# Optimization experiments

Hardware: AMD Instinct MI355X
Metric: run time of the kernel (lower is better)

Reference implementation:

```python
import jax, jax.numpy as jnp
import numpy as np
from jax import lax

B = 64; C_IN = 3; HW = 64
D_INPUT = 256; D_MODEL = 1024; HEADS = 8; HEAD_DIM = D_INPUT // HEADS
ITERS = 16; MEM_LEN = 25; MEM_HID = 64
N_SYNCH = 256; OUT_DIMS = 1000
SYNCH_SIZE = N_SYNCH * (N_SYNCH + 1) // 2  # 32896
TRIU_I, TRIU_J = np.triu_indices(N_SYNCH)
EPS = 1e-5
SCALE = float(1.0 / np.sqrt(HEAD_DIM))


def setup_inputs() -> dict:
    key = jax.random.key(0)
    ks = iter(jax.random.split(key, 64))
    def rn(shape, scale=0.02):
        return jax.random.normal(next(ks), shape, jnp.float32) * scale
    inp = {
        'x': jax.random.normal(next(ks), (B, C_IN, HW, HW), jnp.float32),
        # backbone: conv(3->256) + BN, conv(256->256) + BN
        'conv1_w': rn((D_INPUT, C_IN, 3, 3)), 'conv1_b': jnp.zeros((D_INPUT,), jnp.float32),
        'bn1_g': jnp.ones((D_INPUT,), jnp.float32), 'bn1_b': jnp.zeros((D_INPUT,), jnp.float32),
        'conv2_w': rn((D_INPUT, D_INPUT, 3, 3)), 'conv2_b': jnp.zeros((D_INPUT,), jnp.float32),
        'bn2_g': jnp.ones((D_INPUT,), jnp.float32), 'bn2_b': jnp.zeros((D_INPUT,), jnp.float32),
        # kv projection + LayerNorm
        'kv_w': rn((D_INPUT, D_INPUT)), 'kv_b': jnp.zeros((D_INPUT,), jnp.float32),
        'ln_kv_g': jnp.ones((D_INPUT,), jnp.float32), 'ln_kv_b': jnp.zeros((D_INPUT,), jnp.float32),
        # q projection from action-synch representation
        'q_w': rn((SYNCH_SIZE, D_INPUT)), 'q_b': jnp.zeros((D_INPUT,), jnp.float32),
        # multihead attention in/out projections
        'wq': rn((D_INPUT, D_INPUT)), 'bq': jnp.zeros((D_INPUT,), jnp.float32),
        'wk': rn((D_INPUT, D_INPUT)), 'bk': jnp.zeros((D_INPUT,), jnp.float32),
        'wv': rn((D_INPUT, D_INPUT)), 'bv': jnp.zeros((D_INPUT,), jnp.float32),
        'wo': rn((D_INPUT, D_INPUT)), 'bo_p': jnp.zeros((D_INPUT,), jnp.float32),
        # synapses: Linear(d_input+d_model -> 2*d_model) + GLU + LayerNorm
        'syn_w': rn((D_INPUT + D_MODEL, 2 * D_MODEL)), 'syn_b': jnp.zeros((2 * D_MODEL,), jnp.float32),
        'ln_syn_g': jnp.ones((D_MODEL,), jnp.float32), 'ln_syn_b': jnp.zeros((D_MODEL,), jnp.float32),
        # trace processor (per-neuron SuperLinear MLPs)
        'tp1_w': rn((MEM_LEN, 2 * MEM_HID, D_MODEL), 0.1), 'tp1_b': jnp.zeros((1, D_MODEL, 2 * MEM_HID), jnp.float32),
        'tp2_w': rn((MEM_HID, 2, D_MODEL), 0.1), 'tp2_b': jnp.zeros((1, D_MODEL, 2), jnp.float32),
        # output projector
        'out_w': rn((SYNCH_SIZE, OUT_DIMS)), 'out_b': jnp.zeros((OUT_DIMS,), jnp.float32),
        # recurrent initial state + decay params
        'start_act': rn((D_MODEL,), 0.03), 'start_trace': rn((D_MODEL, MEM_LEN), 0.03),
        'decay_a': jax.random.uniform(next(ks), (SYNCH_SIZE,), jnp.float32) * 0.5,
        'decay_o': jax.random.uniform(next(ks), (SYNCH_SIZE,), jnp.float32) * 0.5,
    }
    return inp


def _conv(x, w, b):
    y = lax.conv_general_dilated(x, w, (1, 1), 'SAME', dimension_numbers=('NCHW', 'OIHW', 'NCHW'))
    return y + b[None, :, None, None]

def _pool(x):
    return lax.reduce_window(x, -jnp.inf, lax.max, (1, 1, 2, 2), (1, 1, 2, 2), 'VALID')

def _bn(x, g, b):
    m = x.mean((0, 2, 3), keepdims=True)
    v = ((x - m) ** 2).mean((0, 2, 3), keepdims=True)
    return g[None, :, None, None] * (x - m) * lax.rsqrt(v + EPS) + b[None, :, None, None]

def _ln(x, g, b):
    m = x.mean(-1, keepdims=True)
    v = ((x - m) ** 2).mean(-1, keepdims=True)
    return g * (x - m) * lax.rsqrt(v + EPS) + b

def _glu(t):
    a, g = jnp.split(t, 2, axis=-1)
    return a * jax.nn.sigmoid(g)

def _synch(sel, alpha, beta, r):
    # outer[:, i, j] == sel[:, i] * sel[:, j] for upper-triangular (i, j)
    pp = sel[:, TRIU_I] * sel[:, TRIU_J]
    alpha = r * alpha + pp
    beta = r * beta + 1.0
    return alpha * lax.rsqrt(beta), alpha, beta


def reference(x, conv1_w, conv1_b, bn1_g, bn1_b, conv2_w, conv2_b, bn2_g, bn2_b,
              kv_w, kv_b, ln_kv_g, ln_kv_b, q_w, q_b, wq, bq, wk, bk, wv, bv, wo, bo_p,
              syn_w, syn_b, ln_syn_g, ln_syn_b, tp1_w, tp1_b, tp2_w, tp2_b,
              out_w, out_b, start_act, start_trace, decay_a, decay_o):
    # backbone -> kv features [B, S, D_INPUT], S = 16*16
    h = _pool(jax.nn.relu(_bn(_conv(x, conv1_w, conv1_b), bn1_g, bn1_b)))
    h = _pool(jax.nn.relu(_bn(_conv(h, conv2_w, conv2_b), bn2_g, bn2_b)))
    feat = h.reshape(B, D_INPUT, -1).transpose(0, 2, 1)
    kv = _ln(feat @ kv_w + kv_b, ln_kv_g, ln_kv_b)
    kh = (kv @ wk + bk).reshape(B, -1, HEADS, HEAD_DIM)
    vh = (kv @ wv + bv).reshape(B, -1, HEADS, HEAD_DIM)

    r_a = jnp.exp(-decay_a)[None]
    r_o = jnp.exp(-decay_o)[None]
    act0 = jnp.broadcast_to(start_act, (B, D_MODEL))
    trace0 = jnp.broadcast_to(start_trace, (B, D_MODEL, MEM_LEN))
    sel0 = act0[:, :N_SYNCH]
    ao0 = sel0[:, TRIU_I] * sel0[:, TRIU_J]
    bo0 = jnp.ones_like(ao0)
    aa0 = jnp.zeros((B, SYNCH_SIZE), x.dtype)  # r*0 + pp reproduces the None-init branch
    ba0 = jnp.zeros((B, SYNCH_SIZE), x.dtype)
    so0 = jnp.zeros((B, SYNCH_SIZE), x.dtype)

    def step(carry, _):
        trace, act, aa, ba, ao, bo, _so = carry
        sa, aa, ba = _synch(act[:, -N_SYNCH:], aa, ba, r_a)
        q = sa @ q_w + q_b
        qh = (q @ wq + bq).reshape(B, HEADS, HEAD_DIM)
        scores = jnp.einsum('bhd,bshd->bhs', qh, kh) * SCALE
        w = jax.nn.softmax(scores, axis=-1)
        attn = jnp.einsum('bhs,bshd->bhd', w, vh).reshape(B, D_INPUT) @ wo + bo_p
        pre = jnp.concatenate([attn, act], axis=-1)
        state = _ln(_glu(pre @ syn_w + syn_b), ln_syn_g, ln_syn_b)
        trace = jnp.concatenate([trace[:, :, 1:], state[:, :, None]], axis=-1)
        hmid = _glu(jnp.einsum('bdm,mhd->bdh', trace, tp1_w) + tp1_b)  # [B, D, MEM_HID]
        act = _glu(jnp.einsum('bdm,mhd->bdh', hmid, tp2_w) + tp2_b)[..., 0]  # [B, D]
        so, ao, bo = _synch(act[:, :N_SYNCH], ao, bo, r_o)
        pred = so @ out_w + out_b
        lp = jax.nn.log_softmax(pred, axis=-1)
        ne = -(jnp.exp(lp) * lp).sum(-1) / jnp.log(jnp.float32(OUT_DIMS))
        cert = jnp.stack([ne, 1.0 - ne], axis=-1)
        return (trace, act, aa, ba, ao, bo, so), (pred, cert)

    carry, (preds, certs) = lax.scan(step, (trace0, act0, aa0, ba0, ao0, bo0, so0), None, length=ITERS)
    predictions = jnp.transpose(preds, (1, 2, 0))   # [B, OUT_DIMS, ITERS]
    certainties = jnp.transpose(certs, (1, 2, 0))   # [B, 2, ITERS]
    return predictions, certainties, carry[6]
```

## Files before the change

### kernel.cpp

```cpp
#include <hip/hip_runtime.h>

#define SYNCH 32896
#define EPS 1e-5f

__device__ __forceinline__ float wave_sum(float v) {
#pragma unroll
  for (int o = 32; o; o >>= 1) v += __shfl_xor(v, o, 64);
  return v;
}
__device__ __forceinline__ float wave_max(float v) {
#pragma unroll
  for (int o = 32; o; o >>= 1) v = fmaxf(v, __shfl_xor(v, o, 64));
  return v;
}
__device__ __forceinline__ float block_sum(float v, float* red, int t) {
  v = wave_sum(v);
  __syncthreads();
  if ((t & 63) == 0) red[t >> 6] = v;
  __syncthreads();
  return red[0] + red[1] + red[2] + red[3];
}
__device__ __forceinline__ float block_max(float v, float* red, int t) {
  v = wave_max(v);
  __syncthreads();
  if ((t & 63) == 0) red[t >> 6] = v;
  __syncthreads();
  return fmaxf(fmaxf(red[0], red[1]), fmaxf(red[2], red[3]));
}
__device__ __forceinline__ float sigm(float x) { return 1.f / (1.f + __expf(-x)); }

__device__ __forceinline__ float conv1_at(const float* __restrict__ x,
                                          const float* __restrict__ w,
                                          int b, int o, int y, int xx) {
  float acc = 0.f;
#pragma unroll
  for (int c = 0; c < 3; ++c) {
    const float* xp = x + ((b * 3 + c) << 12);
    const float* wp = w + (o * 3 + c) * 9;
#pragma unroll
    for (int ky = 0; ky < 3; ++ky) {
      int iy = y + ky - 1;
      if ((unsigned)iy > 63u) continue;
#pragma unroll
      for (int kx = 0; kx < 3; ++kx) {
        int ix = xx + kx - 1;
        if ((unsigned)ix > 63u) continue;
        acc += xp[(iy << 6) + ix] * wp[ky * 3 + kx];
      }
    }
  }
  return acc;
}

__global__ __launch_bounds__(256) void conv1_stats_k(const float* __restrict__ x,
    const float* __restrict__ w, const float* __restrict__ bias, float* __restrict__ st) {
  int idx = blockIdx.x * 256 + threadIdx.x;
  int xx = idx & 63, yy = (idx >> 6) & 63, o = (idx >> 12) & 255, b = idx >> 20;
  float v = bias[o] + conv1_at(x, w, b, o, yy, xx);
  __shared__ float red[4];
  float s = block_sum(v, red, threadIdx.x);
  float s2 = block_sum(v * v, red, threadIdx.x);
  if (threadIdx.x == 0) { atomicAdd(&st[o], s); atomicAdd(&st[256 + o], s2); }
}

__global__ void bn_final_k(const float* st, float* m, float* inv, float n) {
  int o = threadIdx.x;
  float mu = st[o] / n;
  float var = st[256 + o] / n - mu * mu;
  m[o] = mu; inv[o] = rsqrtf(var + EPS);
}

__global__ __launch_bounds__(256) void conv1_pool_k(const float* __restrict__ x,
    const float* __restrict__ w, const float* __restrict__ bias,
    const float* __restrict__ m, const float* __restrict__ inv,
    const float* __restrict__ g, const float* __restrict__ bb,
    float* __restrict__ h1) {
  int idx = blockIdx.x * 256 + threadIdx.x;
  int xx = idx & 31, yy = (idx >> 5) & 31, o = (idx >> 10) & 255, b = idx >> 18;
  float mu = m[o], iv = inv[o], gg = g[o], be = bb[o], bi = bias[o];
  float best = -1e30f;
#pragma unroll
  for (int py = 0; py < 2; ++py)
#pragma unroll
    for (int px = 0; px < 2; ++px) {
      float v = bi + conv1_at(x, w, b, o, 2 * yy + py, 2 * xx + px);
      v = fmaxf(gg * (v - mu) * iv + be, 0.f);
      best = fmaxf(best, v);
    }
  h1[((b * 256 + o) * 32 + yy) * 32 + xx] = best;
}

__global__ __launch_bounds__(256) void conv2_k(const float* __restrict__ h1,
    const float* __restrict__ w, const float* __restrict__ bias, float* __restrict__ y2) {
  __shared__ __align__(16) float tile[34 * 36];
  int b = blockIdx.x >> 4;
  int og = blockIdx.x & 15;
  int t = threadIdx.x;
  int o = og * 16 + (t >> 4);
  int l = t & 15;
  int x0 = (l & 3) * 8, y0 = (l >> 2) * 8;
  float acc[8][8];
#pragma unroll
  for (int i = 0; i < 8; ++i)
#pragma unroll
    for (int j = 0; j < 8; ++j) acc[i][j] = 0.f;
  for (int c = 0; c < 256; ++c) {
    __syncthreads();
    for (int i = t; i < 34 * 34; i += 256) {
      int r = i / 34, cc = i - r * 34;
      int iy = r - 1, ix = cc - 1;
      float v = 0.f;
      if ((unsigned)iy < 32u && (unsigned)ix < 32u) v = h1[((b * 256 + c) * 32 + iy) * 32 + ix];
      tile[r * 36 + cc] = v;
    }
    __syncthreads();
    const float* wp = w + (o * 256 + c) * 9;
    float w0 = wp[0], w1 = wp[1], w2 = wp[2], w3 = wp[3], w4 = wp[4],
          w5 = wp[5], w6 = wp[6], w7 = wp[7], w8 = wp[8];
#pragma unroll
    for (int r = 0; r < 10; ++r) {
      const float* trow = &tile[(y0 + r) * 36 + x0];
      float4 A = *(const float4*)trow;
      float4 Bq = *(const float4*)(trow + 4);
      float4 Cq = *(const float4*)(trow + 8);
      float v[12] = {A.x, A.y, A.z, A.w, Bq.x, Bq.y, Bq.z, Bq.w, Cq.x, Cq.y, Cq.z, Cq.w};
#pragma unroll
      for (int i = 0; i < 8; ++i) {
        int ky = r - i;
        if (ky < 0 || ky > 2) continue;
        float wk0 = (ky == 0) ? w0 : (ky == 1) ? w3 : w6;
        float wk1 = (ky == 0) ? w1 : (ky == 1) ? w4 : w7;
        float wk2 = (ky == 0) ? w2 : (ky == 1) ? w5 : w8;
#pragma unroll
        for (int j = 0; j < 8; ++j)
          acc[i][j] += v[j] * wk0 + v[j + 1] * wk1 + v[j + 2] * wk2;
      }
    }
  }
  float bo = bias[o];
#pragma unroll
  for (int i = 0; i < 8; ++i)
#pragma unroll
    for (int j = 0; j < 8; ++j)
      y2[((b * 256 + o) * 32 + y0 + i) * 32 + x0 + j] = acc[i][j] + bo;
}

__global__ __launch_bounds__(256) void bn2_stats_k(const float* __restrict__ y2,
    float* __restrict__ m2, float* __restrict__ i2) {
  int o = blockIdx.x, t = threadIdx.x;
  float s = 0.f, s2 = 0.f;
  for (int i = t; i < 65536; i += 256) {
    int b = i >> 10, sp = i & 1023;
    float v = y2[((b << 8) + o) * 1024 + sp];
    s += v; s2 += v * v;
  }
  __shared__ float red[4];
  float S = block_sum(s, red, t);
  float S2 = block_sum(s2, red, t);
  if (t == 0) {
    float mu = S / 65536.f;
    m2[o] = mu;
    i2[o] = rsqrtf(S2 / 65536.f - mu * mu + EPS);
  }
}

__global__ __launch_bounds__(256) void pool2_k(const float* __restrict__ y2,
    const float* __restrict__ m2, const float* __restrict__ i2,
    const float* __restrict__ g, const float* __restrict__ bb, float* __restrict__ feat) {
  int idx = blockIdx.x * 256 + threadIdx.x;
  int d = idx & 255, s = (idx >> 8) & 255, b = idx >> 16;
  int yy = s >> 4, xx = s & 15;
  const float* base = y2 + ((size_t)(b * 256 + d) << 10);
  float mu = m2[d], iv = i2[d], gg = g[d], be = bb[d];
  float best = -1e30f;
#pragma unroll
  for (int py = 0; py < 2; ++py)
#pragma unroll
    for (int px = 0; px < 2; ++px) {
      float v = base[(2 * yy + py) * 32 + 2 * xx + px];
      v = fmaxf(gg * (v - mu) * iv + be, 0.f);
      best = fmaxf(best, v);
    }
  feat[(b * 256 + s) * 256 + d] = best;
}

__global__ __launch_bounds__(256) void gemm4x4_k(const float* __restrict__ A, int lda,
    const float* __restrict__ A2, int lda2, int K1,
    const float* __restrict__ W, const float* __restrict__ bias,
    float* __restrict__ C, int M, int N, int K, int kchunk, int atomic) {
  __shared__ __align__(16) float As[16][68];
  __shared__ __align__(16) float Ws[16][68];
  int tx = threadIdx.x, ty = threadIdx.y;
  int tid = ty * 16 + tx;
  int n0 = blockIdx.x * 64, m0 = blockIdx.y * 64;
  int k_lo = blockIdx.z * kchunk;
  int k_hi = min(K, k_lo + kchunk);
  float acc[4][4];
#pragma unroll
  for (int i = 0; i < 4; ++i)
#pragma unroll
    for (int j = 0; j < 4; ++j) acc[i][j] = 0.f;
  for (int k0 = k_lo; k0 < k_hi; k0 += 16) {
    __syncthreads();
#pragma unroll
    for (int q = 0; q < 4; ++q) {
      int r = (tid >> 4) + q * 16, c = tid & 15;
      int mm = m0 + r, kk = k0 + c;
      float a = 0.f;
      if (mm < M && kk < k_hi) a = (kk < K1) ? A[mm * lda + kk] : A2[mm * lda2 + kk - K1];
      As[c][r] = a;
    }
#pragma unroll
    for (int q = 0; q < 4; ++q) {
      int kk = (tid >> 6) + q * 4, nn = tid & 63;
      int kg = k0 + kk, n = n0 + nn;
      Ws[kk][nn] = (kg < k_hi && n < N) ? W[kg * N + n] : 0.f;
    }
    __syncthreads();
#pragma unroll
    for (int kk = 0; kk < 16; ++kk) {
      float4 av = *(const float4*)&As[kk][ty * 4];
      float4 wv = *(const float4*)&Ws[kk][tx * 4];
      float av4[4] = {av.x, av.y, av.z, av.w};
      float wv4[4] = {wv.x, wv.y, wv.z, wv.w};
#pragma unroll
      for (int i = 0; i < 4; ++i)
#pragma unroll
        for (int j = 0; j < 4; ++j) acc[i][j] += av4[i] * wv4[j];
    }
  }
#pragma unroll
  for (int i = 0; i < 4; ++i) {
    int mm = m0 + ty * 4 + i;
    if (mm >= M) continue;
#pragma unroll
    for (int j = 0; j < 4; ++j) {
      int n = n0 + tx * 4 + j;
      if (n >= N) continue;
      float v = acc[i][j];
      if (bias && blockIdx.z == 0) v += bias[n];
      if (atomic) atomicAdd(&C[mm * N + n], v);
      else C[mm * N + n] = v;
    }
  }
}

__global__ __launch_bounds__(256) void ln256_k(float* __restrict__ x,
    const float* __restrict__ g, const float* __restrict__ b) {
  int row = blockIdx.x, t = threadIdx.x;
  float v = x[row * 256 + t];
  __shared__ float red[4];
  float mu = block_sum(v, red, t) * (1.f / 256.f);
  float d = v - mu;
  float var = block_sum(d * d, red, t) * (1.f / 256.f);
  float rs = rsqrtf(var + EPS);
  x[row * 256 + t] = g[t] * d * rs + b[t];
}

__global__ __launch_bounds__(256) void skinny_k(const float* __restrict__ AT,
    const float* __restrict__ W, float* __restrict__ part, int K, int N, int kchunk) {
  int n = blockIdx.x * 256 + threadIdx.x;
  int nc = min(n, N - 1);
  int kc = blockIdx.y;
  int k_lo = kc * kchunk, k_hi = min(K, k_lo + kchunk);
  float acc[64];
#pragma unroll
  for (int b = 0; b < 64; ++b) acc[b] = 0.f;
  for (int k = k_lo; k < k_hi; ++k) {
    float w = W[k * N + nc];
    const float* __restrict__ ap = AT + (k << 6);
#pragma unroll
    for (int b = 0; b < 64; ++b) acc[b] += ap[b] * w;
  }
  if (n < N) {
#pragma unroll
    for (int b = 0; b < 64; ++b) part[(kc * 64 + b) * N + n] = acc[b];
  }
}

__global__ __launch_bounds__(256) void skred_k(const float* __restrict__ part,
    const float* __restrict__ bias, float* __restrict__ C, int N, int nch) {
  int n = blockIdx.x * 256 + threadIdx.x;
  int b = blockIdx.y;
  if (n >= N) return;
  float s = bias[n];
  for (int kc = 0; kc < nch; ++kc) s += part[(kc * 64 + b) * N + n];
  C[b * N + n] = s;
}

__global__ __launch_bounds__(256) void attn_k(const float* __restrict__ qh,
    const float* __restrict__ kh, const float* __restrict__ vh, float* __restrict__ out) {
  int b = blockIdx.x >> 3, h = blockIdx.x & 7;
  int t = threadIdx.x;
  __shared__ float qs[32];
  __shared__ float wgt[256];
  __shared__ float pv[256];
  __shared__ float red[4];
  if (t < 32) qs[t] = qh[b * 256 + h * 32 + t];
  __syncthreads();
  const float4* kp = (const float4*)(kh + ((size_t)((b * 256 + t) * 8 + h)) * 32);
  float sc = 0.f;
#pragma unroll
  for (int q = 0; q < 8; ++q) {
    float4 k4 = kp[q];
    sc += k4.x * qs[4 * q] + k4.y * qs[4 * q + 1] + k4.z * qs[4 * q + 2] + k4.w * qs[4 * q + 3];
  }
  sc *= 0.17677669529663687f;
  float M = block_max(sc, red, t);
  float e = __expf(sc - M);
  float S = block_sum(e, red, t);
  wgt[t] = e / S;
  __syncthreads();
  int d = t & 31, grp = t >> 5;
  float a = 0.f;
  for (int s = grp; s < 256; s += 8)
    a += wgt[s] * vh[((size_t)((b * 256 + s) * 8 + h)) * 32 + d];
  pv[t] = a;
  __syncthreads();
  if (t < 32) {
    float s = 0.f;
#pragma unroll
    for (int g2 = 0; g2 < 8; ++g2) s += pv[g2 * 32 + t];
    out[b * 256 + h * 32 + t] = s;
  }
}

__global__ __launch_bounds__(256) void gluln_k(const float* __restrict__ gt,
    const float* __restrict__ g, const float* __restrict__ bb,
    float* __restrict__ trace, int slot) {
  int b = blockIdx.x, t = threadIdx.x;
  float v[4];
  float s = 0.f;
#pragma unroll
  for (int i = 0; i < 4; ++i) {
    int d = i * 256 + t;
    float a = gt[b * 2048 + d];
    float gg = gt[b * 2048 + 1024 + d];
    v[i] = a * sigm(gg);
    s += v[i];
  }
  __shared__ float red[4];
  float mu = block_sum(s, red, t) * (1.f / 1024.f);
  float s2 = 0.f;
#pragma unroll
  for (int i = 0; i < 4; ++i) { float d0 = v[i] - mu; s2 += d0 * d0; }
  float var = block_sum(s2, red, t) * (1.f / 1024.f);
  float rs = rsqrtf(var + EPS);
  float* tr = trace + (b * 25 + slot) * 1024;
#pragma unroll
  for (int i = 0; i < 4; ++i) {
    int d = i * 256 + t;
    tr[d] = g[d] * (v[i] - mu) * rs + bb[d];
  }
}

#define FMA4(dst, sv, wv) dst.x += sv.x*wv.x; dst.y += sv.y*wv.y; dst.z += sv.z*wv.z; dst.w += sv.w*wv.w;
__global__ __launch_bounds__(256) void tp1_k(const float* __restrict__ trace,
    const float* __restrict__ w1, const float* __restrict__ b1,
    float* __restrict__ hmid, int toff) {
  int gx = blockIdx.x * 256 + threadIdx.x;
  int d4 = gx & 255;
  int hg = (gx >> 8) & 7;
  int bp = gx >> 11;
  int b0 = bp * 2;
  int h0 = hg * 8;
  float4 acc[2][2][8];
#pragma unroll
  for (int a = 0; a < 2; ++a)
#pragma unroll
    for (int c = 0; c < 2; ++c)
#pragma unroll
      for (int u = 0; u < 8; ++u) acc[a][c][u] = make_float4(0.f, 0.f, 0.f, 0.f);
  for (int m = 0; m < 25; ++m) {
    int pm = toff + m; if (pm >= 25) pm -= 25;
    float4 t0 = *(const float4*)&trace[((b0) * 25 + pm) * 1024 + d4 * 4];
    float4 t1 = *(const float4*)&trace[((b0 + 1) * 25 + pm) * 1024 + d4 * 4];
    const float* wb = w1 + m * 131072 + d4 * 4;
#pragma unroll
    for (int u = 0; u < 8; ++u) {
      float4 wa = *(const float4*)&wb[(h0 + u) * 1024];
      float4 wg = *(const float4*)&wb[(64 + h0 + u) * 1024];
      FMA4(acc[0][0][u], t0, wa); FMA4(acc[0][1][u], t0, wg);
      FMA4(acc[1][0][u], t1, wa); FMA4(acc[1][1][u], t1, wg);
    }
  }
  int dbase = d4 * 4;
#pragma unroll
  for (int u = 0; u < 8; ++u) {
    int h = h0 + u;
#pragma unroll
    for (int bb2 = 0; bb2 < 2; ++bb2) {
      float4 av = acc[bb2][0][u], gv = acc[bb2][1][u];
      av.x += b1[(dbase + 0) * 128 + h];      av.y += b1[(dbase + 1) * 128 + h];
      av.z += b1[(dbase + 2) * 128 + h];      av.w += b1[(dbase + 3) * 128 + h];
      gv.x += b1[(dbase + 0) * 128 + 64 + h]; gv.y += b1[(dbase + 1) * 128 + 64 + h];
      gv.z += b1[(dbase + 2) * 128 + 64 + h]; gv.w += b1[(dbase + 3) * 128 + 64 + h];
      float4 hm;
      hm.x = av.x * sigm(gv.x); hm.y = av.y * sigm(gv.y);
      hm.z = av.z * sigm(gv.z); hm.w = av.w * sigm(gv.w);
      *(float4*)&hmid[((b0 + bb2) * 64 + h) * 1024 + dbase] = hm;
    }
  }
}

__global__ __launch_bounds__(256) void tp2_k(const float* __restrict__ hmid,
    const float* __restrict__ w2, const float* __restrict__ b2, float* __restrict__ act) {
  int gx = blockIdx.x * 256 + threadIdx.x;
  int d = gx & 1023, b = gx >> 10;
  float a = b2[d * 2], gg = b2[d * 2 + 1];
  for (int h = 0; h < 64; ++h) {
    float hm = hmid[(b * 64 + h) * 1024 + d];
    a += hm * w2[(h * 2) * 1024 + d];
    gg += hm * w2[(h * 2 + 1) * 1024 + d];
  }
  act[gx] = a * sigm(gg);
}

__global__ void selT_k(const float* __restrict__ act, float* __restrict__ selT, int off) {
  int gx = blockIdx.x * 256 + threadIdx.x;
  int b = gx & 63, i = gx >> 6;
  selT[gx] = act[b * 1024 + off + i];
}

__global__ __launch_bounds__(256) void synch_k(const float* __restrict__ selT,
    const int* __restrict__ I, const int* __restrict__ J, const float* __restrict__ r,
    float* __restrict__ al, float* __restrict__ be, float* __restrict__ outT) {
  int gx = blockIdx.x * 256 + threadIdx.x;
  int b = gx & 63, p = gx >> 6;
  float pp = selT[(I[p] << 6) + b] * selT[(J[p] << 6) + b];
  float rr = r[p];
  float a = rr * al[gx] + pp;
  float bt = rr * be[gx] + 1.f;
  al[gx] = a; be[gx] = bt;
  outT[gx] = a * rsqrtf(bt);
}

__global__ __launch_bounds__(256) void entropy_k(const float* __restrict__ pred,
    float* __restrict__ dout, int t) {
  int b = blockIdx.x, tid = threadIdx.x;
  __shared__ float sp[1000];
  __shared__ float red[4];
  float mx = -1e30f;
  for (int i = tid; i < 1000; i += 256) {
    float v = pred[b * 1000 + i];
    sp[i] = v;
    mx = fmaxf(mx, v);
  }
  float M = block_max(mx, red, tid);
  float se = 0.f;
  for (int i = tid; i < 1000; i += 256) se += __expf(sp[i] - M);
  float S = block_sum(se, red, tid);
  float lse = M + __logf(S);
  float acc = 0.f;
  for (int i = tid; i < 1000; i += 256) {
    float lp = sp[i] - lse;
    acc += __expf(lp) * lp;
    dout[b * 16000 + i * 16 + t] = sp[i];
  }
  float E = block_sum(acc, red, tid);
  if (tid == 0) {
    float ne = -E * (1.f / 6.907755278982137f);
    dout[1024000 + b * 32 + t] = ne;
    dout[1024000 + b * 32 + 16 + t] = 1.f - ne;
  }
}

__global__ void triu_k(int* __restrict__ I, int* __restrict__ J) {
  int p = blockIdx.x * 256 + threadIdx.x;
  if (p >= SYNCH) return;
  float pf = (float)p;
  int i = (int)floorf((513.f - sqrtf(513.f * 513.f - 8.f * pf)) * 0.5f);
  i = max(0, min(255, i));
  while (i > 0 && i * (513 - i) / 2 > p) --i;
  while (i < 255 && (i + 1) * (513 - (i + 1)) / 2 <= p) ++i;
  I[p] = i;
  J[p] = i + (p - i * (513 - i) / 2);
}

__global__ void initr_k(const float* da, const float* dc, float* ra, float* ro) {
  int p = blockIdx.x * 256 + threadIdx.x;
  if (p >= SYNCH) return;
  ra[p] = __expf(-da[p]);
  ro[p] = __expf(-dc[p]);
}

__global__ void initact_k(const float* sa, float* act) {
  int gx = blockIdx.x * 256 + threadIdx.x;
  act[gx] = sa[gx & 1023];
}

__global__ void inittrace_k(const float* st, float* trace) {
  int r = blockIdx.x * 256 + threadIdx.x;
  int b = blockIdx.y;
  int m = r >> 10, d = r & 1023;
  trace[(b * 25 + m) * 1024 + d] = st[d * 25 + m];
}

__global__ void initsynch_k(const int* __restrict__ I, const int* __restrict__ J,
    const float* __restrict__ sa, float* aa, float* ba, float* ao, float* bo) {
  int gx = blockIdx.x * 256 + threadIdx.x;
  int p = gx >> 6;
  aa[gx] = 0.f; ba[gx] = 0.f;
  ao[gx] = sa[I[p]] * sa[J[p]];
  bo[gx] = 1.f;
}

__global__ void soout_k(const float* __restrict__ soT, float* __restrict__ dout) {
  int p = blockIdx.x * 256 + threadIdx.x;
  int b = blockIdx.y;
  if (p >= SYNCH) return;
  dout[1026048 + b * 32896 + p] = soT[(p << 6) + b];
}

extern "C" void kernel_launch(void* const* d_in, const int* in_sizes, int n_in,
                              void* d_out, int out_size, void* d_ws, size_t ws_size,
                              hipStream_t stream) {
  (void)in_sizes; (void)n_in; (void)out_size; (void)ws_size;
  const float* x      = (const float*)d_in[0];
  const float* c1w    = (const float*)d_in[1];
  const float* c1b    = (const float*)d_in[2];
  const float* bn1g   = (const float*)d_in[3];
  const float* bn1b   = (const float*)d_in[4];
  const float* c2w    = (const float*)d_in[5];
  const float* c2b    = (const float*)d_in[6];
  const float* bn2g   = (const float*)d_in[7];
  const float* bn2b   = (const float*)d_in[8];
  const float* kvw    = (const float*)d_in[9];
  const float* kvb    = (const float*)d_in[10];
  const float* lnkvg  = (const float*)d_in[11];
  const float* lnkvb  = (const float*)d_in[12];
  const float* qw     = (const float*)d_in[13];
  const float* qb     = (const float*)d_in[14];
  const float* wq     = (const float*)d_in[15];
  const float* bq     = (const float*)d_in[16];
  const float* wk     = (const float*)d_in[17];
  const float* bk     = (const float*)d_in[18];
  const float* wv     = (const float*)d_in[19];
  const float* bv     = (const float*)d_in[20];
  const float* wo     = (const float*)d_in[21];
  const float* bop    = (const float*)d_in[22];
  const float* synw   = (const float*)d_in[23];
  const float* synb   = (const float*)d_in[24];
  const float* lnsg   = (const float*)d_in[25];
  const float* lnsb   = (const float*)d_in[26];
  const float* t1w    = (const float*)d_in[27];
  const float* t1b    = (const float*)d_in[28];
  const float* t2w    = (const float*)d_in[29];
  const float* t2b    = (const float*)d_in[30];
  const float* outw   = (const float*)d_in[31];
  const float* outb   = (const float*)d_in[32];
  const float* sact   = (const float*)d_in[33];
  const float* strace = (const float*)d_in[34];
  const float* dca    = (const float*)d_in[35];
  const float* dco    = (const float*)d_in[36];
  float* out = (float*)d_out;

  float* W = (float*)d_ws;
  size_t off = 0;
  auto alloc = [&](size_t n) { float* p = W + off; off += (n + 63) & ~(size_t)63; return p; };
  float* h1    = alloc(16777216);
  float* y2    = alloc(16777216);
  float* feat  = alloc(4194304);
  float* kv    = alloc(4194304);
  float* kh    = alloc(4194304);
  float* vh    = alloc(4194304);
  float* st    = alloc(512);
  float* m1    = alloc(256); float* i1 = alloc(256);
  float* m2    = alloc(256); float* i2 = alloc(256);
  int*   tI    = (int*)alloc(32896);
  int*   tJ    = (int*)alloc(32896);
  float* ra    = alloc(32896);
  float* ro    = alloc(32896);
  float* aa    = alloc(2105344);
  float* ba    = alloc(2105344);
  float* ao    = alloc(2105344);
  float* bo    = alloc(2105344);
  float* saT   = alloc(2105344);
  float* soT   = alloc(2105344);
  float* act   = alloc(65536);
  float* trace = alloc(1638400);
  float* selT  = alloc(16384);
  float* q     = alloc(16384);
  float* qh    = alloc(16384);
  float* ath   = alloc(16384);
  float* ato   = alloc(16384);
  float* glut  = alloc(131072);
  float* hmid  = alloc(4194304);
  float* pred  = alloc(64000);
  float* part  = alloc(8256000);

  dim3 thr(16, 16);

  hipMemsetAsync(st, 0, 512 * sizeof(float), stream);
  conv1_stats_k<<<262144, 256, 0, stream>>>(x, c1w, c1b, st);
  bn_final_k<<<1, 256, 0, stream>>>(st, m1, i1, 262144.f);
  conv1_pool_k<<<65536, 256, 0, stream>>>(x, c1w, c1b, m1, i1, bn1g, bn1b, h1);
  conv2_k<<<1024, 256, 0, stream>>>(h1, c2w, c2b, y2);
  bn2_stats_k<<<256, 256, 0, stream>>>(y2, m2, i2);
  pool2_k<<<16384, 256, 0, stream>>>(y2, m2, i2, bn2g, bn2b, feat);
  gemm4x4_k<<<dim3(4, 256, 1), thr, 0, stream>>>(feat, 256, feat, 256, 256, kvw, kvb, kv, 16384, 256, 256, 256, 0);
  ln256_k<<<16384, 256, 0, stream>>>(kv, lnkvg, lnkvb);
  gemm4x4_k<<<dim3(4, 256, 1), thr, 0, stream>>>(kv, 256, kv, 256, 256, wk, bk, kh, 16384, 256, 256, 256, 0);
  gemm4x4_k<<<dim3(4, 256, 1), thr, 0, stream>>>(kv, 256, kv, 256, 256, wv, bv, vh, 16384, 256, 256, 256, 0);

  triu_k<<<129, 256, 0, stream>>>(tI, tJ);
  initr_k<<<129, 256, 0, stream>>>(dca, dco, ra, ro);
  initact_k<<<256, 256, 0, stream>>>(sact, act);
  inittrace_k<<<dim3(100, 64), 256, 0, stream>>>(strace, trace);
  initsynch_k<<<8224, 256, 0, stream>>>(tI, tJ, sact, aa, ba, ao, bo);

  for (int t = 0; t < 16; ++t) {
    selT_k<<<64, 256, 0, stream>>>(act, selT, 768);
    synch_k<<<8224, 256, 0, stream>>>(selT, tI, tJ, ra, aa, ba, saT);
    skinny_k<<<dim3(1, 129), 256, 0, stream>>>(saT, qw, part, 32896, 256, 256);
    skred_k<<<dim3(1, 64), 256, 0, stream>>>(part, qb, q, 256, 129);
    gemm4x4_k<<<dim3(4, 1, 1), thr, 0, stream>>>(q, 256, q, 256, 256, wq, bq, qh, 64, 256, 256, 256, 0);
    attn_k<<<512, 256, 0, stream>>>(qh, kh, vh, ath);
    gemm4x4_k<<<dim3(4, 1, 1), thr, 0, stream>>>(ath, 256, ath, 256, 256, wo, bop, ato, 64, 256, 256, 256, 0);
    hipMemsetAsync(glut, 0, 131072 * sizeof(float), stream);
    gemm4x4_k<<<dim3(32, 1, 8), thr, 0, stream>>>(ato, 256, act, 1024, 256, synw, synb, glut, 64, 2048, 1280, 160, 1);
    gluln_k<<<64, 256, 0, stream>>>(glut, lnsg, lnsb, trace, t);
    tp1_k<<<256, 256, 0, stream>>>(trace, t1w, t1b, hmid, t + 1);
    tp2_k<<<256, 256, 0, stream>>>(hmid, t2w, t2b, act);
    selT_k<<<64, 256, 0, stream>>>(act, selT, 0);
    synch_k<<<8224, 256, 0, stream>>>(selT, tI, tJ, ro, ao, bo, soT);
    skinny_k<<<dim3(4, 129), 256, 0, stream>>>(soT, outw, part, 32896, 1000, 256);
    skred_k<<<dim3(4, 64), 256, 0, stream>>>(part, outb, pred, 1000, 129);
    entropy_k<<<64, 256, 0, stream>>>(pred, out, t);
  }
  soout_k<<<dim3(129, 64), 256, 0, stream>>>(soT, out);
}
```

Before: 13.71 ms.

## Fold q/out projections into weights, fuse reductions, switch synch layout to row-major

Precomputes q_w@wq and wo@syn_w (plus folded biases) once before the loop, so the per-step q projection and attention-output GEMMs disappear. Split-K partial sums are now reduced inside the consumer kernels (attention, GLU-LN, prediction entropy) instead of separate reduce kernels, atomics and memsets. The synch state moves to batch-major layout, and the beta accumulator is replaced by a closed-form geometric series, which removes two state arrays and the selT kernels. The skinny GEMM now reads batch-major activations with 8-way k unrolling, and the buffers are re-aliased into the backbone scratch. The price is a large one-time precompute GEMM over 32896x256 and less coalesced per-batch activation reads in the skinny kernel.

```diff
diff --git a/kernel.cpp b/kernel.cpp
--- a/kernel.cpp
+++ b/kernel.cpp
@@ -187,7 +187,7 @@
 __global__ __launch_bounds__(256) void gemm4x4_k(const float* __restrict__ A, int lda,
     const float* __restrict__ A2, int lda2, int K1,
     const float* __restrict__ W, const float* __restrict__ bias,
-    float* __restrict__ C, int M, int N, int K, int kchunk, int atomic) {
+    float* __restrict__ C, int M, int N, int K, int kchunk, int mode) {
   __shared__ __align__(16) float As[16][68];
   __shared__ __align__(16) float Ws[16][68];
   int tx = threadIdx.x, ty = threadIdx.y;
@@ -207,14 +207,14 @@
       int r = (tid >> 4) + q * 16, c = tid & 15;
       int mm = m0 + r, kk = k0 + c;
       float a = 0.f;
-      if (mm < M && kk < k_hi) a = (kk < K1) ? A[mm * lda + kk] : A2[mm * lda2 + kk - K1];
+      if (mm < M && kk < k_hi) a = (kk < K1) ? A[(size_t)mm * lda + kk] : A2[(size_t)mm * lda2 + kk - K1];
       As[c][r] = a;
     }
 #pragma unroll
     for (int q = 0; q < 4; ++q) {
       int kk = (tid >> 6) + q * 4, nn = tid & 63;
       int kg = k0 + kk, n = n0 + nn;
-      Ws[kk][nn] = (kg < k_hi && n < N) ? W[kg * N + n] : 0.f;
+      Ws[kk][nn] = (kg < k_hi && n < N) ? W[(size_t)kg * N + n] : 0.f;
     }
     __syncthreads();
 #pragma unroll
@@ -238,9 +238,12 @@
       int n = n0 + tx * 4 + j;
       if (n >= N) continue;
       float v = acc[i][j];
-      if (bias && blockIdx.z == 0) v += bias[n];
-      if (atomic) atomicAdd(&C[mm * N + n], v);
-      else C[mm * N + n] = v;
+      if (mode == 2) {
+        C[((size_t)blockIdx.z * M + mm) * N + n] = v;
+      } else {
+        if (bias && blockIdx.z == 0) v += bias[n];
+        C[(size_t)mm * N + n] = v;
+      }
     }
   }
 }
@@ -257,7 +260,7 @@
   x[row * 256 + t] = g[t] * d * rs + b[t];
 }
 
-__global__ __launch_bounds__(256) void skinny_k(const float* __restrict__ AT,
+__global__ __launch_bounds__(256) void skinny_k(const float* __restrict__ A,
     const float* __restrict__ W, float* __restrict__ part, int K, int N, int kchunk) {
   int n = blockIdx.x * 256 + threadIdx.x;
   int nc = min(n, N - 1);
@@ -266,37 +269,53 @@
   float acc[64];
 #pragma unroll
   for (int b = 0; b < 64; ++b) acc[b] = 0.f;
-  for (int k = k_lo; k < k_hi; ++k) {
-    float w = W[k * N + nc];
-    const float* __restrict__ ap = AT + (k << 6);
-#pragma unroll
-    for (int b = 0; b < 64; ++b) acc[b] += ap[b] * w;
+  int k = k_lo;
+  for (; k + 8 <= k_hi; k += 8) {
+    float w[8];
+#pragma unroll
+    for (int j = 0; j < 8; ++j) w[j] = W[(size_t)(k + j) * N + nc];
+#pragma unroll
+    for (int b = 0; b < 64; ++b) {
+      const float* __restrict__ ap = A + b * K + k;
+#pragma unroll
+      for (int j = 0; j < 8; ++j) acc[b] = fmaf(ap[j], w[j], acc[b]);
+    }
+  }
+  for (; k < k_hi; ++k) {
+    float w0 = W[(size_t)k * N + nc];
+#pragma unroll
+    for (int b = 0; b < 64; ++b) acc[b] = fmaf(A[b * K + k], w0, acc[b]);
   }
   if (n < N) {
 #pragma unroll
-    for (int b = 0; b < 64; ++b) part[(kc * 64 + b) * N + n] = acc[b];
-  }
-}
-
-__global__ __launch_bounds__(256) void skred_k(const float* __restrict__ part,
-    const float* __restrict__ bias, float* __restrict__ C, int N, int nch) {
-  int n = blockIdx.x * 256 + threadIdx.x;
-  int b = blockIdx.y;
-  if (n >= N) return;
-  float s = bias[n];
-  for (int kc = 0; kc < nch; ++kc) s += part[(kc * 64 + b) * N + n];
-  C[b * N + n] = s;
-}
-
-__global__ __launch_bounds__(256) void attn_k(const float* __restrict__ qh,
-    const float* __restrict__ kh, const float* __restrict__ vh, float* __restrict__ out) {
+    for (int b = 0; b < 64; ++b) part[(size_t)(kc * 64 + b) * N + n] = acc[b];
+  }
+}
+
+__global__ __launch_bounds__(256) void attn_k(const float* __restrict__ part_q,
+    const float* __restrict__ qbq, const float* __restrict__ kh,
+    const float* __restrict__ vh, float* __restrict__ out, int nkc) {
   int b = blockIdx.x >> 3, h = blockIdx.x & 7;
   int t = threadIdx.x;
+  __shared__ float q8[256];
   __shared__ float qs[32];
   __shared__ float wgt[256];
   __shared__ float pv[256];
   __shared__ float red[4];
-  if (t < 32) qs[t] = qh[b * 256 + h * 32 + t];
+  {
+    int d = t & 31, g = t >> 5;
+    float s = 0.f;
+    for (int kc = g; kc < nkc; kc += 8)
+      s += part_q[(size_t)(kc * 64 + b) * 256 + h * 32 + d];
+    q8[t] = s;
+  }
+  __syncthreads();
+  if (t < 32) {
+    float s = qbq[h * 32 + t];
+#pragma unroll
+    for (int g = 0; g < 8; ++g) s += q8[g * 32 + t];
+    qs[t] = s;
+  }
   __syncthreads();
   const float4* kp = (const float4*)(kh + ((size_t)((b * 256 + t) * 8 + h)) * 32);
   float sc = 0.f;
@@ -325,7 +344,8 @@
   }
 }
 
-__global__ __launch_bounds__(256) void gluln_k(const float* __restrict__ gt,
+__global__ __launch_bounds__(256) void gluln_k(const float* __restrict__ part2,
+    const float* __restrict__ biasyn,
     const float* __restrict__ g, const float* __restrict__ bb,
     float* __restrict__ trace, int slot) {
   int b = blockIdx.x, t = threadIdx.x;
@@ -334,8 +354,14 @@
 #pragma unroll
   for (int i = 0; i < 4; ++i) {
     int d = i * 256 + t;
-    float a = gt[b * 2048 + d];
-    float gg = gt[b * 2048 + 1024 + d];
+    float a = biasyn[d];
+    float gg = biasyn[1024 + d];
+#pragma unroll
+    for (int z = 0; z < 8; ++z) {
+      const float* p = part2 + (size_t)(z * 64 + b) * 2048;
+      a += p[d];
+      gg += p[1024 + d];
+    }
     v[i] = a * sigm(gg);
     s += v[i];
   }
@@ -416,35 +442,38 @@
   act[gx] = a * sigm(gg);
 }
 
-__global__ void selT_k(const float* __restrict__ act, float* __restrict__ selT, int off) {
-  int gx = blockIdx.x * 256 + threadIdx.x;
-  int b = gx & 63, i = gx >> 6;
-  selT[gx] = act[b * 1024 + off + i];
-}
-
-__global__ __launch_bounds__(256) void synch_k(const float* __restrict__ selT,
-    const int* __restrict__ I, const int* __restrict__ J, const float* __restrict__ r,
-    float* __restrict__ al, float* __restrict__ be, float* __restrict__ outT) {
-  int gx = blockIdx.x * 256 + threadIdx.x;
-  int b = gx & 63, p = gx >> 6;
-  float pp = selT[(I[p] << 6) + b] * selT[(J[p] << 6) + b];
-  float rr = r[p];
-  float a = rr * al[gx] + pp;
-  float bt = rr * be[gx] + 1.f;
-  al[gx] = a; be[gx] = bt;
-  outT[gx] = a * rsqrtf(bt);
-}
-
-__global__ __launch_bounds__(256) void entropy_k(const float* __restrict__ pred,
-    float* __restrict__ dout, int t) {
+__global__ __launch_bounds__(256) void synch_k(const float* __restrict__ act,
+    const int* __restrict__ I, const int* __restrict__ J,
+    const float* __restrict__ decay, int off, int n, int has_init,
+    float* __restrict__ al, float* __restrict__ so) {
+  int p = blockIdx.x * 256 + threadIdx.x;
+  if (p >= SYNCH) return;
+  int b = blockIdx.y;
+  const float* arow = act + b * 1024 + off;
+  float pp = arow[I[p]] * arow[J[p]];
+  float d = decay[p];
+  float r = __expf(-d);
+  size_t idx = (size_t)b * SYNCH + p;
+  float a = r * al[idx] + pp;
+  al[idx] = a;
+  float em1d = expm1f(-d);
+  float em1nd = expm1f(-(float)n * d);
+  float beta = (em1d == 0.f) ? (float)n : em1nd / em1d;
+  if (has_init) beta += em1nd + 1.f;
+  so[idx] = a * rsqrtf(beta);
+}
+
+__global__ __launch_bounds__(256) void predent_k(const float* __restrict__ part,
+    const float* __restrict__ bias, float* __restrict__ dout, int nkc, int t) {
   int b = blockIdx.x, tid = threadIdx.x;
   __shared__ float sp[1000];
   __shared__ float red[4];
   float mx = -1e30f;
   for (int i = tid; i < 1000; i += 256) {
-    float v = pred[b * 1000 + i];
-    sp[i] = v;
-    mx = fmaxf(mx, v);
+    float s = bias[i];
+    for (int kc = 0; kc < nkc; ++kc) s += part[(size_t)(kc * 64 + b) * 1000 + i];
+    sp[i] = s;
+    mx = fmaxf(mx, s);
   }
   float M = block_max(mx, red, tid);
   float se = 0.f;
@@ -477,13 +506,6 @@
   J[p] = i + (p - i * (513 - i) / 2);
 }
 
-__global__ void initr_k(const float* da, const float* dc, float* ra, float* ro) {
-  int p = blockIdx.x * 256 + threadIdx.x;
-  if (p >= SYNCH) return;
-  ra[p] = __expf(-da[p]);
-  ro[p] = __expf(-dc[p]);
-}
-
 __global__ void initact_k(const float* sa, float* act) {
   int gx = blockIdx.x * 256 + threadIdx.x;
   act[gx] = sa[gx & 1023];
@@ -497,19 +519,34 @@
 }
 
 __global__ void initsynch_k(const int* __restrict__ I, const int* __restrict__ J,
-    const float* __restrict__ sa, float* aa, float* ba, float* ao, float* bo) {
-  int gx = blockIdx.x * 256 + threadIdx.x;
-  int p = gx >> 6;
-  aa[gx] = 0.f; ba[gx] = 0.f;
-  ao[gx] = sa[I[p]] * sa[J[p]];
-  bo[gx] = 1.f;
-}
-
-__global__ void soout_k(const float* __restrict__ soT, float* __restrict__ dout) {
+    const float* __restrict__ sa, float* aa, float* ao) {
   int p = blockIdx.x * 256 + threadIdx.x;
+  if (p >= SYNCH) return;
   int b = blockIdx.y;
+  size_t idx = (size_t)b * SYNCH + p;
+  aa[idx] = 0.f;
+  ao[idx] = sa[I[p]] * sa[J[p]];
+}
+
+__global__ void soout_k(const float* __restrict__ so, float* __restrict__ dout) {
+  int p = blockIdx.x * 256 + threadIdx.x;
   if (p >= SYNCH) return;
-  dout[1026048 + b * 32896 + p] = soT[(p << 6) + b];
+  int b = blockIdx.y;
+  dout[1026048 + (size_t)b * SYNCH + p] = so[(size_t)b * SYNCH + p];
+}
+
+__global__ void vecbias_k(const float* __restrict__ v, const float* __restrict__ W,
+    const float* __restrict__ bias, float* __restrict__ out, int K, int N) {
+  int n = blockIdx.x * 256 + threadIdx.x;
+  if (n >= N) return;
+  float s = bias[n];
+  for (int k = 0; k < K; ++k) s += v[k] * W[(size_t)k * N + n];
+  out[n] = s;
+}
+
+__global__ void copy_k(const float* __restrict__ src, float* __restrict__ dst, int count) {
+  int i = blockIdx.x * 256 + threadIdx.x;
+  if (i < count) dst[i] = src[i];
 }
 
 extern "C" void kernel_launch(void* const* d_in, const int* in_sizes, int n_in,
@@ -558,36 +595,33 @@
   float* W = (float*)d_ws;
   size_t off = 0;
   auto alloc = [&](size_t n) { float* p = W + off; off += (n + 63) & ~(size_t)63; return p; };
-  float* h1    = alloc(16777216);
-  float* y2    = alloc(16777216);
-  float* feat  = alloc(4194304);
-  float* kv    = alloc(4194304);
-  float* kh    = alloc(4194304);
-  float* vh    = alloc(4194304);
-  float* st    = alloc(512);
-  float* m1    = alloc(256); float* i1 = alloc(256);
-  float* m2    = alloc(256); float* i2 = alloc(256);
-  int*   tI    = (int*)alloc(32896);
-  int*   tJ    = (int*)alloc(32896);
-  float* ra    = alloc(32896);
-  float* ro    = alloc(32896);
-  float* aa    = alloc(2105344);
-  float* ba    = alloc(2105344);
-  float* ao    = alloc(2105344);
-  float* bo    = alloc(2105344);
-  float* saT   = alloc(2105344);
-  float* soT   = alloc(2105344);
-  float* act   = alloc(65536);
-  float* trace = alloc(1638400);
-  float* selT  = alloc(16384);
-  float* q     = alloc(16384);
-  float* qh    = alloc(16384);
-  float* ath   = alloc(16384);
-  float* ato   = alloc(16384);
-  float* glut  = alloc(131072);
-  float* hmid  = alloc(4194304);
-  float* pred  = alloc(64000);
-  float* part  = alloc(8256000);
+  float* h1     = alloc(16777216);
+  float* y2     = alloc(16777216);
+  float* feat   = alloc(4194304);
+  float* st     = alloc(512);
+  float* m1     = alloc(256); float* i1 = alloc(256);
+  float* m2     = alloc(256); float* i2 = alloc(256);
+  int*   tI     = (int*)alloc(32896);
+  int*   tJ     = (int*)alloc(32896);
+  float* aa     = alloc(2105344);
+  float* ao     = alloc(2105344);
+  float* sa     = alloc(2105344);
+  float* so     = alloc(2105344);
+  float* act    = alloc(65536);
+  float* trace  = alloc(1638400);
+  float* part_q = alloc(2097152);
+  float* part2  = alloc(1048576);
+  float* hmid   = alloc(4194304);
+  float* part   = alloc(8192000);
+  float* ath    = alloc(16384);
+  float* qbq    = alloc(256);
+  float* biasyn = alloc(2048);
+
+  float* kv   = h1;
+  float* kh   = h1 + 4194304;
+  float* vh   = h1 + 8388608;
+  float* qwq  = y2;
+  float* wcat = y2 + 8421376;
 
   dim3 thr(16, 16);
 
@@ -602,31 +636,28 @@
   ln256_k<<<16384, 256, 0, stream>>>(kv, lnkvg, lnkvb);
   gemm4x4_k<<<dim3(4, 256, 1), thr, 0, stream>>>(kv, 256, kv, 256, 256, wk, bk, kh, 16384, 256, 256, 256, 0);
   gemm4x4_k<<<dim3(4, 256, 1), thr, 0, stream>>>(kv, 256, kv, 256, 256, wv, bv, vh, 16384, 256, 256, 256, 0);
+  gemm4x4_k<<<dim3(4, 514, 1), thr, 0, stream>>>(qw, 256, qw, 256, 256, wq, nullptr, qwq, 32896, 256, 256, 256, 0);
+  gemm4x4_k<<<dim3(32, 4, 1), thr, 0, stream>>>(wo, 256, wo, 256, 256, synw, nullptr, wcat, 256, 2048, 256, 256, 0);
+  copy_k<<<8192, 256, 0, stream>>>(synw + 524288, wcat + 524288, 2097152);
+  vecbias_k<<<1, 256, 0, stream>>>(qb, wq, bq, qbq, 256, 256);
+  vecbias_k<<<8, 256, 0, stream>>>(bop, synw, synb, biasyn, 256, 2048);
 
   triu_k<<<129, 256, 0, stream>>>(tI, tJ);
-  initr_k<<<129, 256, 0, stream>>>(dca, dco, ra, ro);
   initact_k<<<256, 256, 0, stream>>>(sact, act);
   inittrace_k<<<dim3(100, 64), 256, 0, stream>>>(strace, trace);
-  initsynch_k<<<8224, 256, 0, stream>>>(tI, tJ, sact, aa, ba, ao, bo);
+  initsynch_k<<<dim3(129, 64), 256, 0, stream>>>(tI, tJ, sact, aa, ao);
 
   for (int t = 0; t < 16; ++t) {
-    selT_k<<<64, 256, 0, stream>>>(act, selT, 768);
-    synch_k<<<8224, 256, 0, stream>>>(selT, tI, tJ, ra, aa, ba, saT);
-    skinny_k<<<dim3(1, 129), 256, 0, stream>>>(saT, qw, part, 32896, 256, 256);
-    skred_k<<<dim3(1, 64), 256, 0, stream>>>(part, qb, q, 256, 129);
-    gemm4x4_k<<<dim3(4, 1, 1), thr, 0, stream>>>(q, 256, q, 256, 256, wq, bq, qh, 64, 256, 256, 256, 0);
-    attn_k<<<512, 256, 0, stream>>>(qh, kh, vh, ath);
-    gemm4x4_k<<<dim3(4, 1, 1), thr, 0, stream>>>(ath, 256, ath, 256, 256, wo, bop, ato, 64, 256, 256, 256, 0);
-    hipMemsetAsync(glut, 0, 131072 * sizeof(float), stream);
-    gemm4x4_k<<<dim3(32, 1, 8), thr, 0, stream>>>(ato, 256, act, 1024, 256, synw, synb, glut, 64, 2048, 1280, 160, 1);
-    gluln_k<<<64, 256, 0, stream>>>(glut, lnsg, lnsb, trace, t);
+    synch_k<<<dim3(129, 64), 256, 0, stream>>>(act, tI, tJ, dca, 768, t + 1, 0, aa, sa);
+    skinny_k<<<dim3(1, 128), 256, 0, stream>>>(sa, qwq, part_q, 32896, 256, 257);
+    attn_k<<<512, 256, 0, stream>>>(part_q, qbq, kh, vh, ath, 128);
+    gemm4x4_k<<<dim3(32, 1, 8), thr, 0, stream>>>(ath, 256, act, 1024, 256, wcat, nullptr, part2, 64, 2048, 1280, 160, 2);
+    gluln_k<<<64, 256, 0, stream>>>(part2, biasyn, lnsg, lnsb, trace, t);
     tp1_k<<<256, 256, 0, stream>>>(trace, t1w, t1b, hmid, t + 1);
     tp2_k<<<256, 256, 0, stream>>>(hmid, t2w, t2b, act);
-    selT_k<<<64, 256, 0, stream>>>(act, selT, 0);
-    synch_k<<<8224, 256, 0, stream>>>(selT, tI, tJ, ro, ao, bo, soT);
-    skinny_k<<<dim3(4, 129), 256, 0, stream>>>(soT, outw, part, 32896, 1000, 256);
-    skred_k<<<dim3(4, 64), 256, 0, stream>>>(part, outb, pred, 1000, 129);
-    entropy_k<<<64, 256, 0, stream>>>(pred, out, t);
-  }
-  soout_k<<<dim3(129, 64), 256, 0, stream>>>(soT, out);
-}
+    synch_k<<<dim3(129, 64), 256, 0, stream>>>(act, tI, tJ, dco, 0, t + 1, 1, ao, so);
+    skinny_k<<<dim3(4, 128), 256, 0, stream>>>(so, outw, part, 32896, 1000, 257);
+    predent_k<<<64, 256, 0, stream>>>(part, outb, out, 128, t);
+  }
+  soout_k<<<dim3(129, 64), 256, 0, stream>>>(so, out);
+}
```

New measurement: 16.44 ms. 1.2x slower.
